# Optimization experiments

Hardware: AMD Instinct MI355X
Metric: run time of the kernel (lower is better)

Reference implementation:

```python
import jax, jax.numpy as jnp
import numpy as np

HIDDEN = 1024
HEADS = 16
HEAD_DIM = HIDDEN // HEADS
SCALE = float(np.sqrt(HEAD_DIM))


def setup_inputs() -> dict:
    key = jax.random.key(0)
    ks = jax.random.split(key, 9)
    B, S = 4, 8192
    std = 1.0 / np.sqrt(HIDDEN)
    x = jax.random.normal(ks[0], (B, S, HIDDEN), dtype=jnp.float32)
    Wq = jax.random.normal(ks[1], (HIDDEN, HIDDEN), dtype=jnp.float32) * std
    Wk = jax.random.normal(ks[2], (HIDDEN, HIDDEN), dtype=jnp.float32) * std
    Wv = jax.random.normal(ks[3], (HIDDEN, HIDDEN), dtype=jnp.float32) * std
    Wo = jax.random.normal(ks[4], (HIDDEN, HIDDEN), dtype=jnp.float32) * std
    bq = jax.random.normal(ks[5], (HIDDEN,), dtype=jnp.float32) * std
    bk = jax.random.normal(ks[6], (HIDDEN,), dtype=jnp.float32) * std
    bv = jax.random.normal(ks[7], (HIDDEN,), dtype=jnp.float32) * std
    bo = jax.random.normal(ks[8], (HIDDEN,), dtype=jnp.float32) * std
    return {"x": x, "Wq": Wq, "bq": bq, "Wk": Wk, "bk": bk,
            "Wv": Wv, "bv": bv, "Wo": Wo, "bo": bo}


def reference(x, Wq, bq, Wk, bk, Wv, bv, Wo, bo):
    B, S, E = x.shape
    H, D = HEADS, HEAD_DIM
    # torch nn.Linear: y = x @ W^T + b
    q = (jnp.einsum('bse,fe->bsf', x, Wq) + bq).reshape(B, S, H, D)
    k = (jnp.einsum('bse,fe->bsf', x, Wk) + bk).reshape(B, S, H, D)
    v = (jnp.einsum('bse,fe->bsf', x, Wv) + bv).reshape(B, S, H, D)
    # Faithful to source: NO head transpose, so matmul contracts over head_dim
    # with (B,S) as batch dims -> per-token head-mixing scores [B,S,H,H].
    scores = jnp.einsum('bshd,bsgd->bshg', q, k) / SCALE
    probs = jax.nn.softmax(scores, axis=-1)
    attn = jnp.einsum('bshg,bsgd->bshd', probs, v).reshape(B, S, E)
    return jnp.einsum('bse,fe->bsf', attn, Wo) + bo
```

## Files before the change

### kernel.cpp

```cpp
#include <hip/hip_runtime.h>
#include <hip/hip_bf16.h>
#include <cstdint>
#include <type_traits>

#define GLOBAL_AS __attribute__((address_space(1)))
#define LDS_AS    __attribute__((address_space(3)))

typedef short bf16x8 __attribute__((ext_vector_type(8)));
typedef short short8_t __attribute__((ext_vector_type(8)));
typedef float f32x4  __attribute__((ext_vector_type(4)));

static constexpr int E_DIM = 1024;
static constexpr int HD = 64;
static constexpr int QKV_STRIDE = 3072;
static constexpr int KDIM = 1024;
static constexpr int NT_K = KDIM / 64;
static constexpr int NIT  = NT_K / 2;

__device__ __forceinline__ float b2f(short s) {
    union { unsigned u; float f; } x;
    x.u = ((unsigned)(unsigned short)s) << 16;
    return x.f;
}
__device__ __forceinline__ short f2b(float f) {
    union { float f; unsigned u; } x; x.f = f;
    unsigned r = x.u + 0x7FFF + ((x.u >> 16) & 1);
    return (short)(r >> 16);
}

__global__ __launch_bounds__(256) void k_convert(const float* __restrict__ in,
                                                 short* __restrict__ out, int n4) {
    int i = blockIdx.x * 256 + threadIdx.x;
    if (i >= n4) return;
    float4 v = reinterpret_cast<const float4*>(in)[i];
    short4 o;
    o.x = f2b(v.x); o.y = f2b(v.y); o.z = f2b(v.z); o.w = f2b(v.w);
    reinterpret_cast<short4*>(out)[i] = o;
}

__global__ __launch_bounds__(256) void k_bcat(const float* __restrict__ bq,
                                              const float* __restrict__ bk,
                                              const float* __restrict__ bv,
                                              float* __restrict__ o) {
    int i = blockIdx.x * 256 + threadIdx.x;
    float v = (i < 1024) ? bq[i] : (i < 2048 ? bk[i - 1024] : bv[i - 2048]);
    o[i] = v;
}

template <typename OutT>
__global__ __launch_bounds__(512, 2) void k_gemm256(
    const short* __restrict__ A,
    const short* __restrict__ Bm,
    const float* __restrict__ bias,
    OutT* __restrict__ C,
    int NT_N, int N)
{
    __shared__ short lds[2][2][2][8192];

    const int tid  = threadIdx.x;
    const int lane = tid & 63;
    const int wv   = tid >> 6;
    const int wr   = wv >> 2;
    const int wc   = wv & 3;
    const int frow = lane & 15;
    const int ks   = lane >> 4;

    const int nwg  = gridDim.x;
    const int nper = nwg >> 3;
    const int bid  = blockIdx.x;
    const int swz  = (bid & 7) * nper + (bid >> 3);
    const int m0   = (swz / NT_N) * 256;
    const int n0   = (swz % NT_N) * 256;

    const int c0 = tid, c1 = tid + 512;
    const int r0 = c0 >> 2, z0 = ((c0 & 3) ^ ((c0 >> 3) & 3)) * 8;
    const int r1 = c1 >> 2, z1 = ((c1 & 3) ^ ((c1 >> 3) & 3)) * 8;

#define STAGE(BUF, MAT, KH, BASE, ROW0, KT) do {                                   \
    __builtin_amdgcn_global_load_lds(                                              \
        (const GLOBAL_AS short*)((BASE) + (size_t)((ROW0) + r0) * KDIM +           \
                                 (KT) * 64 + (KH) * 32 + z0),                      \
        (LDS_AS short*)&lds[BUF][MAT][KH][c0 * 8], 16, 0, 0);                      \
    __builtin_amdgcn_global_load_lds(                                              \
        (const GLOBAL_AS short*)((BASE) + (size_t)((ROW0) + r1) * KDIM +           \
                                 (KT) * 64 + (KH) * 32 + z1),                      \
        (LDS_AS short*)&lds[BUF][MAT][KH][c1 * 8], 16, 0, 0);                      \
} while (0)

#define LDA(BUF, KH, R) (*reinterpret_cast<const bf16x8*>(                         \
        &lds[BUF][0][KH][((R) * 4 + (ks ^ (((R) >> 1) & 3))) * 8]))
#define LDB(BUF, KH, R) (*reinterpret_cast<const bf16x8*>(                         \
        &lds[BUF][1][KH][((R) * 4 + (ks ^ (((R) >> 1) & 3))) * 8]))

    f32x4 acc[8][4];
    #pragma unroll
    for (int i = 0; i < 8; ++i)
        #pragma unroll
        for (int j = 0; j < 4; ++j)
            acc[i][j] = (f32x4){0.f, 0.f, 0.f, 0.f};

    bf16x8 af[8], bf0, bf1;

#define PHASE(BUF, KK, NH, WAITE, STAGE_STMT) do {                                 \
    if ((NH) == 0) {                                                               \
        _Pragma("unroll")                                                          \
        for (int mi = 0; mi < 8; ++mi)                                             \
            af[mi] = LDA(BUF, KK, wr * 128 + mi * 16 + frow);                      \
    }                                                                              \
    bf0 = LDB(BUF, KK, wc * 64 + (NH) * 32 + frow);                                \
    bf1 = LDB(BUF, KK, wc * 64 + (NH) * 32 + 16 + frow);                           \
    STAGE_STMT;                                                                    \
    __builtin_amdgcn_s_barrier();                                                  \
    asm volatile("s_waitcnt lgkmcnt(0)" ::: "memory");                             \
    __builtin_amdgcn_s_setprio(1);                                                 \
    _Pragma("unroll")                                                              \
    for (int mi = 0; mi < 8; ++mi) {                                               \
        acc[mi][(NH)*2]   = __builtin_amdgcn_mfma_f32_16x16x32_bf16(               \
                                af[mi], bf0, acc[mi][(NH)*2], 0, 0, 0);            \
        acc[mi][(NH)*2+1] = __builtin_amdgcn_mfma_f32_16x16x32_bf16(               \
                                af[mi], bf1, acc[mi][(NH)*2+1], 0, 0, 0);          \
    }                                                                              \
    __builtin_amdgcn_s_setprio(0);                                                 \
    if (WAITE) asm volatile("s_waitcnt vmcnt(8)" ::: "memory");                    \
    __builtin_amdgcn_s_barrier();                                                  \
} while (0)

    STAGE(0, 0, 0, A,  m0, 0);  STAGE(0, 1, 0, Bm, n0, 0);
    STAGE(0, 0, 1, A,  m0, 0);  STAGE(0, 1, 1, Bm, n0, 0);
    STAGE(1, 0, 0, A,  m0, 1);  STAGE(1, 1, 0, Bm, n0, 1);
    asm volatile("s_waitcnt vmcnt(8)" ::: "memory");
    __builtin_amdgcn_s_barrier();

    for (int it = 0; it < NIT; ++it) {
        const int t1  = 2 * it + 1;
        const int tp2 = (2 * it + 2 < NT_K) ? 2 * it + 2 : NT_K - 1;
        const int tp3 = (2 * it + 3 < NT_K) ? 2 * it + 3 : NT_K - 1;
        PHASE(0, 0, 0, 0, STAGE(1, 0, 1, A,  m0, t1));
        PHASE(0, 0, 1, 1, STAGE(1, 1, 1, Bm, n0, t1));
        PHASE(0, 1, 0, 0, STAGE(0, 0, 0, A,  m0, tp2));
        PHASE(0, 1, 1, 1, STAGE(0, 1, 0, Bm, n0, tp2));
        PHASE(1, 0, 0, 0, STAGE(0, 0, 1, A,  m0, tp2));
        PHASE(1, 0, 1, 1, STAGE(0, 1, 1, Bm, n0, tp2));
        PHASE(1, 1, 0, 0, STAGE(1, 0, 0, A,  m0, tp3));
        PHASE(1, 1, 1, 1, STAGE(1, 1, 0, Bm, n0, tp3));
    }

    asm volatile("s_waitcnt vmcnt(0)" ::: "memory");

    const int crow = (lane >> 4) * 4;
    const int ccol = lane & 15;
    float bv4[4];
    #pragma unroll
    for (int ni = 0; ni < 4; ++ni)
        bv4[ni] = bias[n0 + wc * 64 + ni * 16 + ccol];
    #pragma unroll
    for (int mi = 0; mi < 8; ++mi) {
        #pragma unroll
        for (int r = 0; r < 4; ++r) {
            const size_t rowg = (size_t)(m0 + wr * 128 + mi * 16 + crow + r) * N;
            #pragma unroll
            for (int ni = 0; ni < 4; ++ni) {
                const int col = n0 + wc * 64 + ni * 16 + ccol;
                float v = acc[mi][ni][r] + bv4[ni];
                if constexpr (std::is_same<OutT, float>::value) {
                    C[rowg + col] = v;
                } else {
                    C[rowg + col] = f2b(v);
                }
            }
        }
    }
#undef PHASE
#undef LDA
#undef LDB
#undef STAGE
}

__global__ __launch_bounds__(256) void k_attn(
    const short* __restrict__ QKV, short* __restrict__ O)
{
    __shared__ short Ks[16][1032];
    __shared__ short Vs[16][1032];

    const int tid = threadIdx.x;
    const int tok0 = blockIdx.x * 16;

    for (int i = tid; i < 2048; i += 256) {
        int t = i >> 7;
        int j = i & 127;
        const size_t base = (size_t)(tok0 + t) * QKV_STRIDE;
        *reinterpret_cast<short8_t*>(&Ks[t][j * 8]) =
            *reinterpret_cast<const short8_t*>(&QKV[base + 1024 + j * 8]);
        *reinterpret_cast<short8_t*>(&Vs[t][j * 8]) =
            *reinterpret_cast<const short8_t*>(&QKV[base + 2048 + j * 8]);
    }
    __syncthreads();

    const int tl = tid >> 4;
    const int h  = tid & 15;

    float qf[64];
    const short* qp = QKV + (size_t)(tok0 + tl) * QKV_STRIDE + h * HD;
    #pragma unroll
    for (int i = 0; i < 8; ++i) {
        short8_t v = *reinterpret_cast<const short8_t*>(&qp[i * 8]);
        #pragma unroll
        for (int j = 0; j < 8; ++j) qf[i * 8 + j] = b2f(v[j]);
    }

    float s[16];
    #pragma unroll
    for (int g = 0; g < 16; ++g) {
        float a = 0.f;
        #pragma unroll
        for (int i = 0; i < 8; ++i) {
            short8_t kv = *reinterpret_cast<const short8_t*>(&Ks[tl][g * HD + i * 8]);
            #pragma unroll
            for (int j = 0; j < 8; ++j) a += qf[i * 8 + j] * b2f(kv[j]);
        }
        s[g] = a * 0.125f;
    }
    float mx = s[0];
    #pragma unroll
    for (int g = 1; g < 16; ++g) mx = fmaxf(mx, s[g]);
    float l = 0.f;
    #pragma unroll
    for (int g = 0; g < 16; ++g) { s[g] = __expf(s[g] - mx); l += s[g]; }
    const float inv = 1.f / l;
    #pragma unroll
    for (int g = 0; g < 16; ++g) s[g] *= inv;

    short* op = O + (size_t)(tok0 + tl) * E_DIM + h * HD;
    #pragma unroll
    for (int c = 0; c < 4; ++c) {
        float a[16];
        #pragma unroll
        for (int j = 0; j < 16; ++j) a[j] = 0.f;
        #pragma unroll
        for (int g = 0; g < 16; ++g) {
            short8_t v0 = *reinterpret_cast<const short8_t*>(&Vs[tl][g * HD + c * 16]);
            short8_t v1 = *reinterpret_cast<const short8_t*>(&Vs[tl][g * HD + c * 16 + 8]);
            #pragma unroll
            for (int j = 0; j < 8; ++j) {
                a[j]     += s[g] * b2f(v0[j]);
                a[8 + j] += s[g] * b2f(v1[j]);
            }
        }
        short8_t o0, o1;
        #pragma unroll
        for (int j = 0; j < 8; ++j) { o0[j] = f2b(a[j]); o1[j] = f2b(a[8 + j]); }
        *reinterpret_cast<short8_t*>(&op[c * 16])     = o0;
        *reinterpret_cast<short8_t*>(&op[c * 16 + 8]) = o1;
    }
}

extern "C" void kernel_launch(void* const* d_in, const int* in_sizes, int n_in,
                              void* d_out, int out_size, void* d_ws, size_t ws_size,
                              hipStream_t stream) {
    const float* x  = (const float*)d_in[0];
    const float* Wq = (const float*)d_in[1];
    const float* bq = (const float*)d_in[2];
    const float* Wk = (const float*)d_in[3];
    const float* bk = (const float*)d_in[4];
    const float* Wv = (const float*)d_in[5];
    const float* bv = (const float*)d_in[6];
    const float* Wo = (const float*)d_in[7];
    const float* bo = (const float*)d_in[8];
    float* out = (float*)d_out;

    const int T = in_sizes[0] / E_DIM;
    char* ws = (char*)d_ws;
    const size_t SZ_X    = (size_t)T * E_DIM * 2;
    const size_t SZ_WQKV = (size_t)3 * E_DIM * E_DIM * 2;
    const size_t SZ_W    = (size_t)E_DIM * E_DIM * 2;
    const size_t SZ_B    = 3072 * sizeof(float) + 4096;

    short* xb    = (short*)(ws);
    short* Wqkvb = (short*)(ws + SZ_X);
    short* Wob   = (short*)(ws + SZ_X + SZ_WQKV);
    float* bqkv  = (float*)(ws + SZ_X + SZ_WQKV + SZ_W);
    short* QKVb  = (short*)(ws + SZ_X + SZ_WQKV + SZ_W + SZ_B);
    short* Ab    = xb;

    const int n4x = T * E_DIM / 4;
    const int n4w = E_DIM * E_DIM / 4;
    k_convert<<<dim3((n4x + 255) / 256), dim3(256), 0, stream>>>(x,  xb, n4x);
    k_convert<<<dim3((n4w + 255) / 256), dim3(256), 0, stream>>>(Wq, Wqkvb,                     n4w);
    k_convert<<<dim3((n4w + 255) / 256), dim3(256), 0, stream>>>(Wk, Wqkvb + E_DIM * E_DIM,     n4w);
    k_convert<<<dim3((n4w + 255) / 256), dim3(256), 0, stream>>>(Wv, Wqkvb + 2 * E_DIM * E_DIM, n4w);
    k_convert<<<dim3((n4w + 255) / 256), dim3(256), 0, stream>>>(Wo, Wob, n4w);
    k_bcat<<<dim3(12), dim3(256), 0, stream>>>(bq, bk, bv, bqkv);

    k_gemm256<short><<<dim3((T / 256) * (QKV_STRIDE / 256)), dim3(512), 0, stream>>>(
        xb, Wqkvb, bqkv, QKVb, QKV_STRIDE / 256, QKV_STRIDE);

    k_attn<<<dim3(T / 16), dim3(256), 0, stream>>>(QKVb, Ab);

    k_gemm256<float><<<dim3((T / 256) * (E_DIM / 256)), dim3(512), 0, stream>>>(
        Ab, Wob, bo, out, E_DIM / 256, E_DIM);
}
```

Baseline: 424.8 us.

## Restructure GEMM main loop into 4-slot ring buffer with full k-half phases

The GEMM main loop is reorganized from 8 half-N phases over a 2x2 double buffer into 4 phases per iteration over a 4-slot LDS ring. Each phase loads all A and B fragments for one 32-wide k slice, issues A and B prefetches three slices ahead, and runs 32 MFMAs between barriers. This halves the number of barrier pairs per k step and deepens the prefetch distance, aiming to hide global-load latency better. In exchange each phase holds 12 fragment registers live, and the loop is no longer unrolled.

```diff
diff --git a/kernel.cpp b/kernel.cpp
--- a/kernel.cpp
+++ b/kernel.cpp
@@ -14,8 +14,7 @@
 static constexpr int HD = 64;
 static constexpr int QKV_STRIDE = 3072;
 static constexpr int KDIM = 1024;
-static constexpr int NT_K = KDIM / 64;
-static constexpr int NIT  = NT_K / 2;
+static constexpr int NKH  = KDIM / 32;
 
 __device__ __forceinline__ float b2f(short s) {
     union { unsigned u; float f; } x;
@@ -55,7 +54,7 @@
     OutT* __restrict__ C,
     int NT_N, int N)
 {
-    __shared__ short lds[2][2][2][8192];
+    __shared__ short lds[4][2][8192];
 
     const int tid  = threadIdx.x;
     const int lane = tid & 63;
@@ -76,21 +75,21 @@
     const int r0 = c0 >> 2, z0 = ((c0 & 3) ^ ((c0 >> 3) & 3)) * 8;
     const int r1 = c1 >> 2, z1 = ((c1 & 3) ^ ((c1 >> 3) & 3)) * 8;
 
-#define STAGE(BUF, MAT, KH, BASE, ROW0, KT) do {                                   \
+#define STAGE(REG, MAT, BASE, ROW0, KH) do {                                       \
     __builtin_amdgcn_global_load_lds(                                              \
         (const GLOBAL_AS short*)((BASE) + (size_t)((ROW0) + r0) * KDIM +           \
-                                 (KT) * 64 + (KH) * 32 + z0),                      \
-        (LDS_AS short*)&lds[BUF][MAT][KH][c0 * 8], 16, 0, 0);                      \
+                                 (KH) * 32 + z0),                                  \
+        (LDS_AS short*)&lds[REG][MAT][c0 * 8], 16, 0, 0);                          \
     __builtin_amdgcn_global_load_lds(                                              \
         (const GLOBAL_AS short*)((BASE) + (size_t)((ROW0) + r1) * KDIM +           \
-                                 (KT) * 64 + (KH) * 32 + z1),                      \
-        (LDS_AS short*)&lds[BUF][MAT][KH][c1 * 8], 16, 0, 0);                      \
+                                 (KH) * 32 + z1),                                  \
+        (LDS_AS short*)&lds[REG][MAT][c1 * 8], 16, 0, 0);                          \
 } while (0)
 
-#define LDA(BUF, KH, R) (*reinterpret_cast<const bf16x8*>(                         \
-        &lds[BUF][0][KH][((R) * 4 + (ks ^ (((R) >> 1) & 3))) * 8]))
-#define LDB(BUF, KH, R) (*reinterpret_cast<const bf16x8*>(                         \
-        &lds[BUF][1][KH][((R) * 4 + (ks ^ (((R) >> 1) & 3))) * 8]))
+#define LDA(REG, R) (*reinterpret_cast<const bf16x8*>(                             \
+        &lds[REG][0][((R) * 4 + (ks ^ (((R) >> 1) & 3))) * 8]))
+#define LDB(REG, R) (*reinterpret_cast<const bf16x8*>(                             \
+        &lds[REG][1][((R) * 4 + (ks ^ (((R) >> 1) & 3))) * 8]))
 
     f32x4 acc[8][4];
     #pragma unroll
@@ -99,50 +98,48 @@
         for (int j = 0; j < 4; ++j)
             acc[i][j] = (f32x4){0.f, 0.f, 0.f, 0.f};
 
-    bf16x8 af[8], bf0, bf1;
-
-#define PHASE(BUF, KK, NH, WAITE, STAGE_STMT) do {                                 \
-    if ((NH) == 0) {                                                               \
-        _Pragma("unroll")                                                          \
-        for (int mi = 0; mi < 8; ++mi)                                             \
-            af[mi] = LDA(BUF, KK, wr * 128 + mi * 16 + frow);                      \
-    }                                                                              \
-    bf0 = LDB(BUF, KK, wc * 64 + (NH) * 32 + frow);                                \
-    bf1 = LDB(BUF, KK, wc * 64 + (NH) * 32 + 16 + frow);                           \
-    STAGE_STMT;                                                                    \
+    bf16x8 af[8], bf[4];
+
+#define PHASE(RG, HS) do {                                                         \
+    _Pragma("unroll")                                                              \
+    for (int mi = 0; mi < 8; ++mi)                                                 \
+        af[mi] = LDA(RG, wr * 128 + mi * 16 + frow);                               \
+    _Pragma("unroll")                                                              \
+    for (int ni = 0; ni < 4; ++ni)                                                 \
+        bf[ni] = LDB(RG, wc * 64 + ni * 16 + frow);                                \
+    STAGE((RG + 3) & 3, 0, A,  m0, HS);                                            \
+    STAGE((RG + 3) & 3, 1, Bm, n0, HS);                                            \
     __builtin_amdgcn_s_barrier();                                                  \
     asm volatile("s_waitcnt lgkmcnt(0)" ::: "memory");                             \
     __builtin_amdgcn_s_setprio(1);                                                 \
     _Pragma("unroll")                                                              \
-    for (int mi = 0; mi < 8; ++mi) {                                               \
-        acc[mi][(NH)*2]   = __builtin_amdgcn_mfma_f32_16x16x32_bf16(               \
-                                af[mi], bf0, acc[mi][(NH)*2], 0, 0, 0);            \
-        acc[mi][(NH)*2+1] = __builtin_amdgcn_mfma_f32_16x16x32_bf16(               \
-                                af[mi], bf1, acc[mi][(NH)*2+1], 0, 0, 0);          \
-    }                                                                              \
+    for (int mi = 0; mi < 8; ++mi)                                                 \
+        _Pragma("unroll")                                                          \
+        for (int ni = 0; ni < 4; ++ni)                                             \
+            acc[mi][ni] = __builtin_amdgcn_mfma_f32_16x16x32_bf16(                 \
+                              af[mi], bf[ni], acc[mi][ni], 0, 0, 0);               \
     __builtin_amdgcn_s_setprio(0);                                                 \
-    if (WAITE) asm volatile("s_waitcnt vmcnt(8)" ::: "memory");                    \
+    asm volatile("s_waitcnt vmcnt(8)" ::: "memory");                               \
     __builtin_amdgcn_s_barrier();                                                  \
 } while (0)
 
-    STAGE(0, 0, 0, A,  m0, 0);  STAGE(0, 1, 0, Bm, n0, 0);
-    STAGE(0, 0, 1, A,  m0, 0);  STAGE(0, 1, 1, Bm, n0, 0);
-    STAGE(1, 0, 0, A,  m0, 1);  STAGE(1, 1, 0, Bm, n0, 1);
+    STAGE(0, 0, A, m0, 0);  STAGE(0, 1, Bm, n0, 0);
+    STAGE(1, 0, A, m0, 1);  STAGE(1, 1, Bm, n0, 1);
+    STAGE(2, 0, A, m0, 2);  STAGE(2, 1, Bm, n0, 2);
     asm volatile("s_waitcnt vmcnt(8)" ::: "memory");
     __builtin_amdgcn_s_barrier();
 
-    for (int it = 0; it < NIT; ++it) {
-        const int t1  = 2 * it + 1;
-        const int tp2 = (2 * it + 2 < NT_K) ? 2 * it + 2 : NT_K - 1;
-        const int tp3 = (2 * it + 3 < NT_K) ? 2 * it + 3 : NT_K - 1;
-        PHASE(0, 0, 0, 0, STAGE(1, 0, 1, A,  m0, t1));
-        PHASE(0, 0, 1, 1, STAGE(1, 1, 1, Bm, n0, t1));
-        PHASE(0, 1, 0, 0, STAGE(0, 0, 0, A,  m0, tp2));
-        PHASE(0, 1, 1, 1, STAGE(0, 1, 0, Bm, n0, tp2));
-        PHASE(1, 0, 0, 0, STAGE(0, 0, 1, A,  m0, tp2));
-        PHASE(1, 0, 1, 1, STAGE(0, 1, 1, Bm, n0, tp2));
-        PHASE(1, 1, 0, 0, STAGE(1, 0, 0, A,  m0, tp3));
-        PHASE(1, 1, 1, 1, STAGE(1, 1, 0, Bm, n0, tp3));
+    #pragma unroll 1
+    for (int it = 0; it < NKH / 4; ++it) {
+        const int h = it * 4;
+        const int s0 = (h + 3 < NKH) ? h + 3 : NKH - 1;
+        const int s1 = (h + 4 < NKH) ? h + 4 : NKH - 1;
+        const int s2 = (h + 5 < NKH) ? h + 5 : NKH - 1;
+        const int s3 = (h + 6 < NKH) ? h + 6 : NKH - 1;
+        PHASE(0, s0);
+        PHASE(1, s1);
+        PHASE(2, s2);
+        PHASE(3, s3);
     }
 
     asm volatile("s_waitcnt vmcnt(0)" ::: "memory");
```

New measurement: 431.7 us. About the same (+1.6%).
